# Kernel tuning notes

Measured on AMD Instinct MI355X. Metric: run time of the kernel, lower is better.

Reference implementation:

```python
import jax, jax.numpy as jnp
import numpy as np

D_NUM = 4      # domain_num
N_ES = 2       # n_expert_specific per domain
N_SH = 4       # total shared experts (n_expert_shared_list = [1,1,1,1])
DIN = 512      # input_dims
H = 256        # expert_params dims[-1]
B = 16384      # batch
NEG_INF = -jnp.inf


def setup_inputs() -> dict:
    key = jax.random.key(0)
    ks = jax.random.split(key, 10)
    s = 1.0 / np.sqrt(DIN)
    x_list = jax.random.normal(ks[0], (D_NUM + 1, B, DIN), jnp.float32)
    sim_domain = jax.random.randint(ks[1], (D_NUM, 2), 0, D_NUM, jnp.int32)
    W_spec = jax.random.normal(ks[2], (D_NUM, N_ES, DIN, H), jnp.float32) * s
    b_spec = jax.random.normal(ks[3], (D_NUM, N_ES, H), jnp.float32) * 0.01
    W_sh = jax.random.normal(ks[4], (N_SH, DIN, H), jnp.float32) * s
    b_sh = jax.random.normal(ks[5], (N_SH, H), jnp.float32) * 0.01
    W_gate = jax.random.normal(ks[6], (D_NUM, DIN, N_ES + N_SH), jnp.float32) * s
    b_gate = jax.random.normal(ks[7], (D_NUM, N_ES + N_SH), jnp.float32) * 0.01
    W_gate_sh = jax.random.normal(ks[8], (DIN, D_NUM * N_ES + N_SH), jnp.float32) * s
    b_gate_sh = jax.random.normal(ks[9], (D_NUM * N_ES + N_SH,), jnp.float32) * 0.01
    return {"x_list": x_list, "sim_domain": sim_domain, "W_spec": W_spec,
            "b_spec": b_spec, "W_sh": W_sh, "b_sh": b_sh, "W_gate": W_gate,
            "b_gate": b_gate, "W_gate_sh": W_gate_sh, "b_gate_sh": b_gate_sh}


def reference(x_list, sim_domain, W_spec, b_spec, W_sh, b_sh, W_gate, b_gate, W_gate_sh, b_gate_sh):
    xd = x_list[:D_NUM]          # [D, B, DIN] per-domain inputs
    xs = x_list[-1]              # [B, DIN] shared input
    # expert MLPs (single hidden layer, relu, dropout=0/eval)
    spec = jax.nn.relu(jnp.einsum('nbd,nedh->nbeh', xd, W_spec) + b_spec[:, None])  # [D,B,E,H]
    shared = jax.nn.relu(jnp.einsum('bd,edh->beh', xs, W_sh) + b_sh)                # [B,S,H]
    # specific gates: softmax activation inside MLP
    g = jax.nn.softmax(jnp.einsum('nbd,nde->nbe', xd, W_gate) + b_gate[:, None], axis=-1)  # [D,B,E+S]
    # mask shared experts of non-similar domains (expert_ranges[d] = [N_ES + d])
    mem = (sim_domain[:, :, None] == jnp.arange(D_NUM)[None, None, :]).any(axis=1)  # [D,D]
    mask = jnp.concatenate([jnp.zeros((D_NUM, N_ES), jnp.float32),
                            jnp.where(mem, 0.0, NEG_INF)], axis=1)                  # [D,E+S]
    # torch code re-softmaxes the (already softmaxed) gate after adding -inf mask
    g = jax.nn.softmax(g + mask[:, None, :], axis=-1)
    # weighted combine without materializing broadcasted shared experts
    outs = (jnp.einsum('nbe,nbeh->nbh', g[..., :N_ES], spec)
            + jnp.einsum('nbe,beh->nbh', g[..., N_ES:], shared))                    # [D,B,H]
    # shared gate (cur_level < n_level)
    gs = jax.nn.softmax(xs @ W_gate_sh + b_gate_sh, axis=-1)                         # [B,D*E+S]
    all_spec = spec.transpose(1, 0, 2, 3).reshape(spec.shape[1], D_NUM * N_ES, H)    # [B,D*E,H]
    out_sh = (jnp.einsum('be,beh->bh', gs[:, :D_NUM * N_ES], all_spec)
              + jnp.einsum('be,beh->bh', gs[:, D_NUM * N_ES:], shared))             # [B,H]
    return jnp.concatenate([outs, out_sh[None]], axis=0)                             # [D+1,B,H]
```

## Files before the change

### kernel.cpp

```cpp
#include <hip/hip_runtime.h>
#include <cstdint>
#include <cstddef>

#define D_NUM 4
#define N_ES  2
#define N_SH  4
#define DIN   512
#define HDIM  256
#define BB    16384
#define MHALF 8192
#define NMAT  12
#define NGATE 36

typedef __bf16 bf16x8 __attribute__((ext_vector_type(8)));
typedef float  f32x4  __attribute__((ext_vector_type(4)));

__device__ __forceinline__ unsigned short f2bf(float f) {
    union { float f; unsigned u; } v; v.f = f;
    unsigned u = v.u;
    unsigned r = (u + 0x7FFFu + ((u >> 16) & 1u)) >> 16;
    return (unsigned short)r;
}
__device__ __forceinline__ float bf2f(unsigned short u) {
    union { unsigned u; float f; } v; v.u = ((unsigned)u) << 16; return v.f;
}
__device__ __forceinline__ void async16(void* l, const void* g) {
    __builtin_amdgcn_global_load_lds(
        (const __attribute__((address_space(1))) void*)g,
        (__attribute__((address_space(3))) void*)l,
        16, 0, 0);
}

__global__ __launch_bounds__(256) void k_wconv(
    const float* __restrict__ Wspec,
    const float* __restrict__ Wsh,
    unsigned short* __restrict__ WT)
{
    __shared__ unsigned short t[64][65];
    const int mat = blockIdx.z;
    const int k0  = blockIdx.x * 64;
    const int h0  = blockIdx.y * 64;
    const float* src = (mat < 8) ? (Wspec + (size_t)mat * DIN * HDIM)
                                 : (Wsh   + (size_t)(mat - 8) * DIN * HDIM);
    #pragma unroll
    for (int i = 0; i < 16; ++i) {
        int idx = i * 256 + threadIdx.x;
        int r = idx >> 6, c = idx & 63;
        t[r][c] = f2bf(src[(size_t)(k0 + r) * HDIM + h0 + c]);
    }
    __syncthreads();
    #pragma unroll
    for (int i = 0; i < 16; ++i) {
        int idx = i * 256 + threadIdx.x;
        int r = idx >> 6, c = idx & 63;
        WT[(size_t)mat * HDIM * DIN + (size_t)(h0 + r) * DIN + k0 + c] = t[c][r];
    }
}

__global__ __launch_bounds__(256) void k_gwt(
    const float* __restrict__ Wg,
    const float* __restrict__ Wgs,
    float* __restrict__ WgT,
    float* __restrict__ WgsT)
{
    int i = blockIdx.x * 256 + threadIdx.x;
    if (i < 4 * 6 * 512) {
        int n = i / 3072, rem = i % 3072;
        int e = rem >> 9, k = rem & 511;
        WgT[i] = Wg[((size_t)n * DIN + k) * 6 + e];
    }
    if (i < 12 * 512) {
        int e = i >> 9, k = i & 511;
        WgsT[i] = Wgs[(size_t)k * 12 + e];
    }
}

__global__ __launch_bounds__(256) void k_prep(
    const float* __restrict__ x,
    const int*   __restrict__ simdom,
    const float* __restrict__ WgT,
    const float* __restrict__ bg,
    const float* __restrict__ WgsT,
    const float* __restrict__ bgs,
    unsigned short* __restrict__ xbf,
    float* __restrict__ gates)
{
    __shared__ float lgate[4][2][36];
    __shared__ float gsm[4][72];
    const int wave = threadIdx.x >> 6;
    const int lane = threadIdx.x & 63;
    const int row0 = blockIdx.x * 8 + wave * 2;
    const int k0   = lane * 8;

    float4 a0[5], b0[5], a1[5], b1[5];
    #pragma unroll
    for (int m = 0; m < 5; ++m) {
        const float* xp0 = x + ((size_t)m * BB + row0) * DIN + k0;
        a0[m] = ((const float4*)xp0)[0];
        b0[m] = ((const float4*)xp0)[1];
        const float* xp1 = xp0 + DIN;
        a1[m] = ((const float4*)xp1)[0];
        b1[m] = ((const float4*)xp1)[1];
    }
    __builtin_amdgcn_sched_barrier(0);

    #pragma unroll
    for (int m = 0; m < 5; ++m) {
        unsigned short* xbp = xbf + ((size_t)m * BB + row0) * DIN + k0;
        {
            union { unsigned short us[8]; uint4 v; } p0, p1;
            p0.us[0]=f2bf(a0[m].x); p0.us[1]=f2bf(a0[m].y);
            p0.us[2]=f2bf(a0[m].z); p0.us[3]=f2bf(a0[m].w);
            p0.us[4]=f2bf(b0[m].x); p0.us[5]=f2bf(b0[m].y);
            p0.us[6]=f2bf(b0[m].z); p0.us[7]=f2bf(b0[m].w);
            p1.us[0]=f2bf(a1[m].x); p1.us[1]=f2bf(a1[m].y);
            p1.us[2]=f2bf(a1[m].z); p1.us[3]=f2bf(a1[m].w);
            p1.us[4]=f2bf(b1[m].x); p1.us[5]=f2bf(b1[m].y);
            p1.us[6]=f2bf(b1[m].z); p1.us[7]=f2bf(b1[m].w);
            *(uint4*)xbp         = p0.v;
            *(uint4*)(xbp + DIN) = p1.v;
        }
        if (m < 4) {
            float z0[6], z1[6];
            #pragma unroll
            for (int e = 0; e < 6; ++e) {
                const float* wp = WgT + ((size_t)(m * 6 + e)) * DIN + k0;
                float4 wa = ((const float4*)wp)[0], wb = ((const float4*)wp)[1];
                z0[e] = a0[m].x*wa.x + a0[m].y*wa.y + a0[m].z*wa.z + a0[m].w*wa.w
                      + b0[m].x*wb.x + b0[m].y*wb.y + b0[m].z*wb.z + b0[m].w*wb.w;
                z1[e] = a1[m].x*wa.x + a1[m].y*wa.y + a1[m].z*wa.z + a1[m].w*wa.w
                      + b1[m].x*wb.x + b1[m].y*wb.y + b1[m].z*wb.z + b1[m].w*wb.w;
            }
            #pragma unroll
            for (int off = 32; off > 0; off >>= 1)
                #pragma unroll
                for (int e = 0; e < 6; ++e) {
                    z0[e] += __shfl_xor(z0[e], off, 64);
                    z1[e] += __shfl_xor(z1[e], off, 64);
                }
            if (lane == 0) {
                #pragma unroll
                for (int e = 0; e < 6; ++e) lgate[wave][0][m * 6 + e] = z0[e];
            }
            if (lane == 1) {
                #pragma unroll
                for (int e = 0; e < 6; ++e) lgate[wave][1][m * 6 + e] = z1[e];
            }
        } else {
            float z0[12], z1[12];
            #pragma unroll
            for (int e = 0; e < 12; ++e) {
                const float* wp = WgsT + (size_t)e * DIN + k0;
                float4 wa = ((const float4*)wp)[0], wb = ((const float4*)wp)[1];
                z0[e] = a0[m].x*wa.x + a0[m].y*wa.y + a0[m].z*wa.z + a0[m].w*wa.w
                      + b0[m].x*wb.x + b0[m].y*wb.y + b0[m].z*wb.z + b0[m].w*wb.w;
                z1[e] = a1[m].x*wa.x + a1[m].y*wa.y + a1[m].z*wa.z + a1[m].w*wa.w
                      + b1[m].x*wb.x + b1[m].y*wb.y + b1[m].z*wb.z + b1[m].w*wb.w;
            }
            #pragma unroll
            for (int off = 32; off > 0; off >>= 1)
                #pragma unroll
                for (int e = 0; e < 12; ++e) {
                    z0[e] += __shfl_xor(z0[e], off, 64);
                    z1[e] += __shfl_xor(z1[e], off, 64);
                }
            if (lane == 0) {
                #pragma unroll
                for (int e = 0; e < 12; ++e) lgate[wave][0][24 + e] = z0[e];
            }
            if (lane == 1) {
                #pragma unroll
                for (int e = 0; e < 12; ++e) lgate[wave][1][24 + e] = z1[e];
            }
        }
    }

    __builtin_amdgcn_wave_barrier();
    if (lane < 2) {
        const float* lg = lgate[wave][lane];
        float*       go = &gsm[wave][lane * 36];
        #pragma unroll
        for (int n = 0; n < 4; ++n) {
            float z[6];
            #pragma unroll
            for (int e = 0; e < 6; ++e) z[e] = lg[n * 6 + e] + bg[n * 6 + e];
            float mx = z[0];
            #pragma unroll
            for (int e = 1; e < 6; ++e) mx = fmaxf(mx, z[e]);
            float sum = 0.f;
            #pragma unroll
            for (int e = 0; e < 6; ++e) { z[e] = __expf(z[e] - mx); sum += z[e]; }
            float inv = 1.f / sum;
            #pragma unroll
            for (int e = 0; e < 6; ++e) z[e] *= inv;
            int s0 = simdom[n * 2], s1 = simdom[n * 2 + 1];
            float w[6];
            w[0] = z[0]; w[1] = z[1];
            #pragma unroll
            for (int j = 0; j < 4; ++j)
                w[2 + j] = (s0 == j || s1 == j) ? z[2 + j] : -1e30f;
            float mx2 = w[0];
            #pragma unroll
            for (int e = 1; e < 6; ++e) mx2 = fmaxf(mx2, w[e]);
            float sm = 0.f;
            #pragma unroll
            for (int e = 0; e < 6; ++e) { w[e] = __expf(w[e] - mx2); sm += w[e]; }
            float iv = 1.f / sm;
            #pragma unroll
            for (int e = 0; e < 6; ++e) go[n * 6 + e] = w[e] * iv;
        }
        {
            float z[12];
            #pragma unroll
            for (int e = 0; e < 12; ++e) z[e] = lg[24 + e] + bgs[e];
            float mx = z[0];
            #pragma unroll
            for (int e = 1; e < 12; ++e) mx = fmaxf(mx, z[e]);
            float sum = 0.f;
            #pragma unroll
            for (int e = 0; e < 12; ++e) { z[e] = __expf(z[e] - mx); sum += z[e]; }
            float inv = 1.f / sum;
            #pragma unroll
            for (int e = 0; e < 12; ++e) go[24 + e] = z[e] * inv;
        }
    }
    __builtin_amdgcn_wave_barrier();
    for (int j = lane; j < 72; j += 64)
        gates[(size_t)row0 * NGATE + j] = gsm[wave][j];
}

__global__ __launch_bounds__(256) void k_gemm(
    const unsigned short* __restrict__ xbf,
    const unsigned short* __restrict__ WT,
    const float* __restrict__ bspec,
    const float* __restrict__ bsh,
    unsigned short* __restrict__ S,
    int row_base)
{
    __shared__ unsigned short lbuf[16384];

    const int tid  = threadIdx.x;
    const int wave = tid >> 6;
    const int lane = tid & 63;
    const int mat  = blockIdx.y >> 1;
    const int hh0  = (blockIdx.y & 1) * 128;
    const int plane = (mat < 8) ? (mat >> 1) : 4;
    const int lrow0 = blockIdx.x * 128;

    const unsigned short* Abase = xbf + ((size_t)plane * BB + row_base + lrow0) * DIN;
    const unsigned short* Bbase = WT + (size_t)mat * HDIM * DIN + (size_t)hh0 * DIN;

    const unsigned short* gb = (wave < 2) ? Abase : Bbase;
    unsigned goff[8];
    unsigned loff[8];
    {
        int cg = (lane & 7) ^ ((lane >> 3) & 7);
        #pragma unroll
        for (int i = 0; i < 8; ++i) {
            int slot = wave * 8 + i;
            int r = (slot & 15) * 8 + (lane >> 3);
            goff[i] = (unsigned)(r * DIN + cg * 8);
            loff[i] = (unsigned)(slot * 512);
        }
    }

    f32x4 acc[4][4];
    #pragma unroll
    for (int t = 0; t < 4; ++t)
        #pragma unroll
        for (int u = 0; u < 4; ++u)
            acc[t][u] = (f32x4){0.f, 0.f, 0.f, 0.f};

    const int wm = wave >> 1, wn = wave & 1;
    const int arow = lane & 15, quad = lane >> 4;
    int aofs[4], bofs[4];
    #pragma unroll
    for (int t = 0; t < 4; ++t) {
        int r = wm * 64 + t * 16 + arow;
        aofs[t] = r * 64 + (quad ^ (r & 7)) * 8;
    }
    #pragma unroll
    for (int u = 0; u < 4; ++u) {
        int r = wn * 64 + u * 16 + arow;
        bofs[u] = 8192 + r * 64 + (quad ^ (r & 7)) * 8;
    }

    for (int ks = 0; ks < 8; ++ks) {
        __syncthreads();
        #pragma unroll
        for (int i = 0; i < 8; ++i) {
            async16(lbuf + loff[i], gb + goff[i]);
            goff[i] += 64;
        }
        __syncthreads();

        #pragma unroll
        for (int s2 = 0; s2 < 2; ++s2) {
            const int sx = s2 * 32;
            bf16x8 af[4], bv[4];
            #pragma unroll
            for (int t = 0; t < 4; ++t) af[t] = *(const bf16x8*)(lbuf + (aofs[t] ^ sx));
            #pragma unroll
            for (int u = 0; u < 4; ++u) bv[u] = *(const bf16x8*)(lbuf + (bofs[u] ^ sx));
            #pragma unroll
            for (int t = 0; t < 4; ++t)
                #pragma unroll
                for (int u = 0; u < 4; ++u)
                    acc[t][u] = __builtin_amdgcn_mfma_f32_16x16x32_bf16(af[t], bv[u], acc[t][u], 0, 0, 0);
        }
    }

    #pragma unroll
    for (int u = 0; u < 4; ++u) {
        const int h = hh0 + wn * 64 + u * 16 + arow;
        const float bias = (mat < 8) ? bspec[mat * HDIM + h] : bsh[(mat - 8) * HDIM + h];
        #pragma unroll
        for (int t = 0; t < 4; ++t) {
            #pragma unroll
            for (int reg = 0; reg < 4; ++reg) {
                int lr = lrow0 + wm * 64 + t * 16 + quad * 4 + reg;
                float v = fmaxf(acc[t][u][reg] + bias, 0.f);
                S[((size_t)mat * MHALF + lr) * HDIM + h] = f2bf(v);
            }
        }
    }
}

__global__ __launch_bounds__(256) void k_comb(
    const unsigned short* __restrict__ S,
    const float* __restrict__ gates,
    float* __restrict__ out,
    int row_base)
{
    const int h = threadIdx.x;
    const int r0 = blockIdx.x * 4;
    #pragma unroll
    for (int rr = 0; rr < 4; ++rr) {
        const int lr = r0 + rr;
        const int grow = row_base + lr;
        const float* g = gates + (size_t)grow * NGATE;
        float s[NMAT];
        #pragma unroll
        for (int mat = 0; mat < NMAT; ++mat)
            s[mat] = bf2f(S[((size_t)mat * MHALF + lr) * HDIM + h]);
        float o4 = 0.f;
        #pragma unroll
        for (int j = 0; j < 8; ++j) o4 += g[24 + j] * s[j];
        #pragma unroll
        for (int e = 0; e < 4; ++e) o4 += g[32 + e] * s[8 + e];
        #pragma unroll
        for (int n = 0; n < 4; ++n) {
            float on = g[n*6+0]*s[n*2] + g[n*6+1]*s[n*2+1]
                     + g[n*6+2]*s[8] + g[n*6+3]*s[9] + g[n*6+4]*s[10] + g[n*6+5]*s[11];
            out[((size_t)n * BB + grow) * HDIM + h] = on;
        }
        out[((size_t)4 * BB + grow) * HDIM + h] = o4;
    }
}

extern "C" void kernel_launch(void* const* d_in, const int* in_sizes, int n_in,
                              void* d_out, int out_size, void* d_ws, size_t ws_size,
                              hipStream_t stream) {
    const float* x      = (const float*)d_in[0];
    const int*   simdom = (const int*)  d_in[1];
    const float* Wspec  = (const float*)d_in[2];
    const float* bspec  = (const float*)d_in[3];
    const float* Wsh    = (const float*)d_in[4];
    const float* bsh    = (const float*)d_in[5];
    const float* Wg     = (const float*)d_in[6];
    const float* bg     = (const float*)d_in[7];
    const float* Wgs    = (const float*)d_in[8];
    const float* bgs    = (const float*)d_in[9];
    float* out = (float*)d_out;

    uint8_t* ws = (uint8_t*)d_ws;
    unsigned short* xbf  = (unsigned short*)(ws);
    unsigned short* WT   = (unsigned short*)(ws + 83886080ull);
    float*          gts  = (float*)(ws + 87031808ull);
    float*          WgT  = (float*)(ws + 89391104ull);
    float*          WgsT = (float*)(ws + 89440256ull);
    unsigned short* S    = (unsigned short*)(ws + 89464832ull);

    k_wconv<<<dim3(8, 4, 12), 256, 0, stream>>>(Wspec, Wsh, WT);
    k_gwt<<<48, 256, 0, stream>>>(Wg, Wgs, WgT, WgsT);
    k_prep<<<BB / 8, 256, 0, stream>>>(x, simdom, WgT, bg, WgsT, bgs, xbf, gts);
    for (int half = 0; half < 2; ++half) {
        int row_base = half * MHALF;
        k_gemm<<<dim3(MHALF / 128, 24), 256, 0, stream>>>(xbf, WT, bspec, bsh, S, row_base);
        k_comb<<<MHALF / 4, 256, 0, stream>>>(S, gts, out, row_base);
    }
}
```

Baseline: 429.1 us.

## Remap GEMM blocks per XCD, stage epilogue through LDS, vectorize combine

The GEMM grid is remapped so that each XCD handles a contiguous group of row tiles across all 24 matrix/half-column slots, which should improve L2 reuse of the A tile. The GEMM epilogue now writes bf16 results into padded shared memory and then stores them with coalesced 16-byte writes instead of scattered 2-byte stores. The combine kernel gives each thread two adjacent columns, using 32-bit loads and float2 stores. k_prep is shrunk to 128-thread blocks. The costs are extra LDS and a barrier in the GEMM epilogue.

```diff
diff --git a/kernel.cpp b/kernel.cpp
--- a/kernel.cpp
+++ b/kernel.cpp
@@ -75,7 +75,7 @@
     }
 }
 
-__global__ __launch_bounds__(256) void k_prep(
+__global__ __launch_bounds__(128) void k_prep(
     const float* __restrict__ x,
     const int*   __restrict__ simdom,
     const float* __restrict__ WgT,
@@ -85,11 +85,11 @@
     unsigned short* __restrict__ xbf,
     float* __restrict__ gates)
 {
-    __shared__ float lgate[4][2][36];
-    __shared__ float gsm[4][72];
+    __shared__ float lgate[2][2][36];
+    __shared__ float gsm[2][72];
     const int wave = threadIdx.x >> 6;
     const int lane = threadIdx.x & 63;
-    const int row0 = blockIdx.x * 8 + wave * 2;
+    const int row0 = blockIdx.x * 4 + wave * 2;
     const int k0   = lane * 8;
 
     float4 a0[5], b0[5], a1[5], b1[5];
@@ -237,15 +237,22 @@
     unsigned short* __restrict__ S,
     int row_base)
 {
-    __shared__ unsigned short lbuf[16384];
+    __shared__ unsigned short lbuf[17408];
 
     const int tid  = threadIdx.x;
     const int wave = tid >> 6;
     const int lane = tid & 63;
-    const int mat  = blockIdx.y >> 1;
-    const int hh0  = (blockIdx.y & 1) * 128;
+
+    const int j    = blockIdx.x + 24 * blockIdx.y;
+    const int xcd  = j & 7;
+    const int slot = j >> 3;
+    const int rg   = xcd * 8 + slot / 24;
+    const int mh   = slot % 24;
+
+    const int mat  = mh >> 1;
+    const int hh0  = (mh & 1) * 128;
     const int plane = (mat < 8) ? (mat >> 1) : 4;
-    const int lrow0 = blockIdx.x * 128;
+    const int lrow0 = rg * 128;
 
     const unsigned short* Abase = xbf + ((size_t)plane * BB + row_base + lrow0) * DIN;
     const unsigned short* Bbase = WT + (size_t)mat * HDIM * DIN + (size_t)hh0 * DIN;
@@ -257,10 +264,10 @@
         int cg = (lane & 7) ^ ((lane >> 3) & 7);
         #pragma unroll
         for (int i = 0; i < 8; ++i) {
-            int slot = wave * 8 + i;
-            int r = (slot & 15) * 8 + (lane >> 3);
+            int slot2 = wave * 8 + i;
+            int r = (slot2 & 15) * 8 + (lane >> 3);
             goff[i] = (unsigned)(r * DIN + cg * 8);
-            loff[i] = (unsigned)(slot * 512);
+            loff[i] = (unsigned)(slot2 * 512);
         }
     }
 
@@ -310,18 +317,31 @@
         }
     }
 
+    __syncthreads();
     #pragma unroll
     for (int u = 0; u < 4; ++u) {
-        const int h = hh0 + wn * 64 + u * 16 + arow;
-        const float bias = (mat < 8) ? bspec[mat * HDIM + h] : bsh[(mat - 8) * HDIM + h];
+        const int hc = wn * 64 + u * 16 + arow;
+        const float bias = (mat < 8) ? bspec[mat * HDIM + hh0 + hc]
+                                     : bsh[(mat - 8) * HDIM + hh0 + hc];
         #pragma unroll
         for (int t = 0; t < 4; ++t) {
+            const int rbase = wm * 64 + t * 16 + quad * 4;
             #pragma unroll
             for (int reg = 0; reg < 4; ++reg) {
-                int lr = lrow0 + wm * 64 + t * 16 + quad * 4 + reg;
                 float v = fmaxf(acc[t][u][reg] + bias, 0.f);
-                S[((size_t)mat * MHALF + lr) * HDIM + h] = f2bf(v);
-            }
+                lbuf[(rbase + reg) * 136 + hc] = f2bf(v);
+            }
+        }
+    }
+    __syncthreads();
+    {
+        unsigned short* Sb = S + ((size_t)mat * MHALF + lrow0) * HDIM + hh0;
+        #pragma unroll
+        for (int i = 0; i < 8; ++i) {
+            int idx = i * 256 + tid;
+            int row = idx >> 4, c8 = idx & 15;
+            *(uint4*)(Sb + (size_t)row * HDIM + c8 * 8) =
+                *(const uint4*)(lbuf + row * 136 + c8 * 8);
         }
     }
 }
@@ -332,29 +352,37 @@
     float* __restrict__ out,
     int row_base)
 {
-    const int h = threadIdx.x;
-    const int r0 = blockIdx.x * 4;
+    const int tid = threadIdx.x;
+    const int h0  = (tid & 127) * 2;
+    const int r0  = blockIdx.x * 8 + (tid >> 7) * 4;
     #pragma unroll
     for (int rr = 0; rr < 4; ++rr) {
         const int lr = r0 + rr;
         const int grow = row_base + lr;
         const float* g = gates + (size_t)grow * NGATE;
-        float s[NMAT];
-        #pragma unroll
-        for (int mat = 0; mat < NMAT; ++mat)
-            s[mat] = bf2f(S[((size_t)mat * MHALF + lr) * HDIM + h]);
-        float o4 = 0.f;
-        #pragma unroll
-        for (int j = 0; j < 8; ++j) o4 += g[24 + j] * s[j];
-        #pragma unroll
-        for (int e = 0; e < 4; ++e) o4 += g[32 + e] * s[8 + e];
+        float sa[NMAT], sb[NMAT];
+        #pragma unroll
+        for (int mat = 0; mat < NMAT; ++mat) {
+            unsigned u = *(const unsigned*)(S + ((size_t)mat * MHALF + lr) * HDIM + h0);
+            sa[mat] = bf2f((unsigned short)(u & 0xFFFFu));
+            sb[mat] = bf2f((unsigned short)(u >> 16));
+        }
+        float o4a = 0.f, o4b = 0.f;
+        #pragma unroll
+        for (int j = 0; j < 8; ++j) { o4a += g[24 + j] * sa[j]; o4b += g[24 + j] * sb[j]; }
+        #pragma unroll
+        for (int e = 0; e < 4; ++e) { o4a += g[32 + e] * sa[8 + e]; o4b += g[32 + e] * sb[8 + e]; }
         #pragma unroll
         for (int n = 0; n < 4; ++n) {
-            float on = g[n*6+0]*s[n*2] + g[n*6+1]*s[n*2+1]
-                     + g[n*6+2]*s[8] + g[n*6+3]*s[9] + g[n*6+4]*s[10] + g[n*6+5]*s[11];
-            out[((size_t)n * BB + grow) * HDIM + h] = on;
-        }
-        out[((size_t)4 * BB + grow) * HDIM + h] = o4;
+            float ona = g[n*6+0]*sa[n*2] + g[n*6+1]*sa[n*2+1]
+                      + g[n*6+2]*sa[8] + g[n*6+3]*sa[9] + g[n*6+4]*sa[10] + g[n*6+5]*sa[11];
+            float onb = g[n*6+0]*sb[n*2] + g[n*6+1]*sb[n*2+1]
+                      + g[n*6+2]*sb[8] + g[n*6+3]*sb[9] + g[n*6+4]*sb[10] + g[n*6+5]*sb[11];
+            float2 o = {ona, onb};
+            *(float2*)(out + ((size_t)n * BB + grow) * HDIM + h0) = o;
+        }
+        float2 o4 = {o4a, o4b};
+        *(float2*)(out + ((size_t)4 * BB + grow) * HDIM + h0) = o4;
     }
 }
 
@@ -383,10 +411,10 @@
 
     k_wconv<<<dim3(8, 4, 12), 256, 0, stream>>>(Wspec, Wsh, WT);
     k_gwt<<<48, 256, 0, stream>>>(Wg, Wgs, WgT, WgsT);
-    k_prep<<<BB / 8, 256, 0, stream>>>(x, simdom, WgT, bg, WgsT, bgs, xbf, gts);
+    k_prep<<<BB / 4, 128, 0, stream>>>(x, simdom, WgT, bg, WgsT, bgs, xbf, gts);
     for (int half = 0; half < 2; ++half) {
         int row_base = half * MHALF;
-        k_gemm<<<dim3(MHALF / 128, 24), 256, 0, stream>>>(xbf, WT, bspec, bsh, S, row_base);
-        k_comb<<<MHALF / 4, 256, 0, stream>>>(S, gts, out, row_base);
-    }
-}
+        k_gemm<<<dim3(24, 64), 256, 0, stream>>>(xbf, WT, bspec, bsh, S, row_base);
+        k_comb<<<MHALF / 8, 256, 0, stream>>>(S, gts, out, row_base);
+    }
+}
```

Result: faster. 410.8 us (-4.3%).
